# Kernel optimization log

Hardware: AMD Instinct MI355X
Metric: run time of the kernel (lower is better)

Reference implementation:

```python
import jax, jax.numpy as jnp
import numpy as np

B, N, HID, H, M = 4, 16384, 512, 8, 32
D = HID // H  # 64


def setup_inputs() -> dict:
    key = jax.random.key(0)
    ks = jax.random.split(key, 8)
    s = 0.02
    return {
        "x": jax.random.normal(ks[0], (B, N, HID), jnp.float32),
        "wkv": jax.random.normal(ks[1], (2 * HID, HID), jnp.float32) * s,
        "bkv": jnp.zeros((2 * HID,), jnp.float32),
        "wtq": jax.random.normal(ks[2], (H, M, D), jnp.float32) * s,
        "alpha1": jnp.ones((H,), jnp.float32),
        "mix1_w": jax.random.normal(ks[3], (H * M, H * M), jnp.float32) * (1.0 / np.sqrt(H * M)),
        "ln1_w": jnp.ones((D,), jnp.float32),
        "ln1_b": jnp.zeros((D,), jnp.float32),
        "wqkv": jax.random.normal(ks[4], (3 * HID, HID), jnp.float32) * s,
        "wout": jax.random.normal(ks[5], (HID, HID), jnp.float32) * s,
        "bout": jnp.zeros((HID,), jnp.float32),
    }


def _layernorm(x, w, b, eps=1e-5):
    mu = x.mean(-1, keepdims=True)
    var = ((x - mu) ** 2).mean(-1, keepdims=True)
    return (x - mu) * jax.lax.rsqrt(var + eps) * w + b


def reference(x, wkv, bkv, wtq, alpha1, mix1_w, ln1_w, ln1_b, wqkv, wout, bout):
    # key/value projection: [B, N, 2*HID]
    kv = x @ wkv.T + bkv
    xk, xv = jnp.split(kv, 2, axis=-1)
    xk = xk.reshape(B, N, H, D).transpose(0, 2, 1, 3)  # b h n d
    xv = xv.reshape(B, N, H, D).transpose(0, 2, 1, 3)
    # slice scores + 1x1 conv head-mixing over the (H*M) channel dim
    scores = jnp.einsum('hmd,bhnd->bhmn', wtq, xk)
    scores = jnp.einsum('oc,bcn->bon', mix1_w, scores.reshape(B, H * M, N)).reshape(B, H, M, N)
    # softmax over the slice dim M (dim=-2)
    sw = jax.nn.softmax(scores * alpha1[:, None, None], axis=-2)  # b h m n
    # weighted reduction to slice tokens, normalized by total weight per slice
    tok = jnp.einsum('bhmn,bhnd->bhmd', sw, xv)
    tok = tok / (sw.sum(axis=-1, keepdims=True) + 1e-5)
    tok = _layernorm(tok, ln1_w, ln1_b)
    tok = tok.transpose(0, 2, 1, 3).reshape(B, M, HID)  # b m (h d)
    # small inner MHA over the M=32 slice tokens
    qkv = tok @ wqkv.T
    q, k, v = jnp.split(qkv, 3, axis=-1)
    q = q.reshape(B, M, H, D).transpose(0, 2, 1, 3)
    k = k.reshape(B, M, H, D).transpose(0, 2, 1, 3)
    v = v.reshape(B, M, H, D).transpose(0, 2, 1, 3)
    dots = jnp.einsum('bhqd,bhkd->bhqk', q, k) * (D ** -0.5)
    attn = jax.nn.softmax(dots, axis=-1)
    out_tok = jnp.einsum('bhqk,bhkd->bhqd', attn, v)
    # broadcast slice tokens back to the N points via slice weights
    out = jnp.einsum('bhmd,bhmn->bhnd', out_tok, sw)
    out = out.transpose(0, 2, 1, 3).reshape(B, N, HID)
    out = out @ wout.T + bout
    return (out, sw, alpha1[:, None, None], jnp.zeros((H, M), jnp.float32), attn)
```

## Files before the change

kernel.cpp:

```cpp
#include <hip/hip_runtime.h>
#include <hip/hip_bf16.h>

#define B_ 4
#define N_ 16384
#define HID_ 512
#define H_ 8
#define M_ 32
#define D_ 64
#define HM_ 256

typedef __hip_bfloat16 bf16;
typedef __bf16 bf16x8 __attribute__((ext_vector_type(8)));
typedef float f32x4 __attribute__((ext_vector_type(4)));

__device__ __forceinline__ void gl_lds16(const bf16* g, bf16* l) {
    __builtin_amdgcn_global_load_lds(
        (const __attribute__((address_space(1))) void*)g,
        (__attribute__((address_space(3))) void*)l, 16, 0, 0);
}

__device__ __forceinline__ int xcd_swz(int lin, int nwg) {
    return (lin & 7) * (nwg >> 3) + (lin >> 3);
}

__device__ __forceinline__ void stage_tile_lin(const bf16* __restrict__ G, long long r0,
        int kk, int ld, bf16* lds, int t) {
    const int l = t & 63, w = t >> 6;
    const int srow = l >> 3;
    const int skel = (l & 7) * 8;
#pragma unroll
    for (int j = 0; j < 4; ++j) {
        int q = j * 4 + w;
        gl_lds16(G + (r0 + q * 8 + srow) * (long long)ld + kk + skel, lds + q * 512);
    }
}

__device__ __forceinline__ void stage_tile_sw(const bf16* __restrict__ G, long long r0,
        int kk, int ld, bf16* lds, int t) {
    const int l = t & 63, w = t >> 6;
    const int srow = l >> 3;
    const int skel = ((l & 7) ^ srow) * 8;
#pragma unroll
    for (int j = 0; j < 4; ++j) {
        int q = j * 4 + w;
        gl_lds16(G + (r0 + q * 8 + srow) * (long long)ld + kk + skel, lds + q * 512);
    }
}

__device__ __forceinline__ void mfma_half(const bf16* As, const bf16* Bs,
        int l, int wm, int wn, f32x4 acc[4][4]) {
#pragma unroll
    for (int ks = 0; ks < 64; ks += 32) {
        bf16x8 af[4], bfr[4];
#pragma unroll
        for (int mf = 0; mf < 4; ++mf)
            af[mf] = *(const bf16x8*)(As + (wm * 64 + mf * 16 + (l & 15)) * 64 + ks + (l >> 4) * 8);
#pragma unroll
        for (int nf = 0; nf < 4; ++nf)
            bfr[nf] = *(const bf16x8*)(Bs + (wn * 64 + nf * 16 + (l & 15)) * 64 + ks + (l >> 4) * 8);
#pragma unroll
        for (int mf = 0; mf < 4; ++mf)
#pragma unroll
            for (int nf = 0; nf < 4; ++nf)
                acc[mf][nf] = __builtin_amdgcn_mfma_f32_16x16x32_bf16(af[mf], bfr[nf], acc[mf][nf], 0, 0, 0);
    }
}

__device__ __forceinline__ void mfma_half_sw(const bf16* As, const bf16* Bs,
        int l, int wm, int wn, f32x4 acc[4][4]) {
    const int l15 = l & 15;
    const int xsw = (l & 7) * 8;
    const int kq = (l >> 4) * 8;
#pragma unroll
    for (int ks = 0; ks < 64; ks += 32) {
        const int ko = (ks + kq) ^ xsw;
        bf16x8 af[4], bfr[4];
#pragma unroll
        for (int mf = 0; mf < 4; ++mf)
            af[mf] = *(const bf16x8*)(As + (wm * 64 + mf * 16 + l15) * 64 + ko);
#pragma unroll
        for (int nf = 0; nf < 4; ++nf)
            bfr[nf] = *(const bf16x8*)(Bs + (wn * 64 + nf * 16 + l15) * 64 + ko);
#pragma unroll
        for (int mf = 0; mf < 4; ++mf)
#pragma unroll
            for (int nf = 0; nf < 4; ++nf)
                acc[mf][nf] = __builtin_amdgcn_mfma_f32_16x16x32_bf16(af[mf], bfr[nf], acc[mf][nf], 0, 0, 0);
    }
}

__device__ __forceinline__ void mfma_core(
        const bf16* __restrict__ Ag, const bf16* __restrict__ Bg,
        long long arow0, int bcol0, int lda, int ldb, int kiters,
        bf16* As, bf16* Bs, f32x4 acc[4][4]) {
    const int t = threadIdx.x;
    const int l = t & 63, w = t >> 6;
    const int wm = w >> 1, wn = w & 1;
    for (int kt = 0; kt < kiters; ++kt) {
        const int kk = kt * 64;
        stage_tile_lin(Ag, arow0, kk, lda, As, t);
        stage_tile_lin(Bg, bcol0, kk, ldb, Bs, t);
        __syncthreads();
        mfma_half(As, Bs, l, wm, wn, acc);
        __syncthreads();
    }
}

template<int NT>
__device__ __forceinline__ void gemm_cnt(
        const bf16* __restrict__ Ag, const bf16* __restrict__ Bg,
        long long arow0, int bcol0, int lda, int ldb,
        bf16 (*As)[8192], bf16 (*Bs)[8192], f32x4 acc[4][4]) {
    const int t = threadIdx.x;
    const int l = t & 63, w = t >> 6;
    const int wm = w >> 1, wn = w & 1;
    stage_tile_sw(Ag, arow0, 0, lda, As[0], t);
    stage_tile_sw(Bg, bcol0, 0, ldb, Bs[0], t);
#pragma unroll
    for (int kt = 0; kt < NT; ++kt) {
        const int cur = kt & 1;
        if (kt + 1 < NT) {
            stage_tile_sw(Ag, arow0, (kt + 1) * 64, lda, As[cur ^ 1], t);
            stage_tile_sw(Bg, bcol0, (kt + 1) * 64, ldb, Bs[cur ^ 1], t);
            asm volatile("s_waitcnt vmcnt(8)" ::: "memory");
        } else {
            asm volatile("s_waitcnt vmcnt(0)" ::: "memory");
        }
        __builtin_amdgcn_s_barrier();
        mfma_half_sw(As[cur], Bs[cur], l, wm, wn, acc);
        __builtin_amdgcn_s_barrier();
    }
}

__global__ __launch_bounds__(256) void k_cast4(const float* __restrict__ s,
        ushort* __restrict__ d) {
    long long i = (long long)blockIdx.x * 256 + threadIdx.x;
    float4 v = reinterpret_cast<const float4*>(s)[i];
    ushort4 o;
    bf16 a0 = __float2bfloat16(v.x), a1 = __float2bfloat16(v.y);
    bf16 a2 = __float2bfloat16(v.z), a3 = __float2bfloat16(v.w);
    o.x = *(ushort*)&a0; o.y = *(ushort*)&a1; o.z = *(ushort*)&a2; o.w = *(ushort*)&a3;
    reinterpret_cast<ushort4*>(d)[i] = o;
}

__global__ __launch_bounds__(256) void k_wfused(const float* __restrict__ mix1,
        const float* __restrict__ wtq, float* __restrict__ wf) {
    const int idx = blockIdx.x * 256 + threadIdx.x;
    const int o = idx >> 9, k = idx & 511;
    const int h = k >> 6, dd = k & 63;
    float s = 0.f;
#pragma unroll
    for (int m = 0; m < 32; ++m)
        s += mix1[(long long)o * 256 + h * 32 + m] * wtq[((long long)h * 32 + m) * 64 + dd];
    wf[(long long)o * 512 + k] = s;
}

__global__ __launch_bounds__(256) void k_wsc(const float* __restrict__ wf,
        const float* __restrict__ wkv, const float* __restrict__ bkv,
        const float* __restrict__ alpha1, bf16* __restrict__ wv_sc,
        float* __restrict__ bias768) {
    __shared__ float wfrow[512];
    __shared__ float red[256];
    const int o = blockIdx.x, t = threadIdx.x;
    wfrow[t] = wf[(long long)o * 512 + t];
    wfrow[t + 256] = wf[(long long)o * 512 + 256 + t];
    __syncthreads();
    const float al = alpha1[o >> 5];
    float a0 = 0.f, a1 = 0.f;
    for (int c = 0; c < 512; ++c) {
        float wv = wfrow[c];
        a0 += wv * wkv[(long long)c * 512 + t];
        a1 += wv * wkv[(long long)c * 512 + t + 256];
    }
    wv_sc[(long long)(512 + o) * 512 + t] = __float2bfloat16(a0 * al);
    wv_sc[(long long)(512 + o) * 512 + t + 256] = __float2bfloat16(a1 * al);
    float p = wfrow[t] * bkv[t] + wfrow[t + 256] * bkv[t + 256];
    red[t] = p; __syncthreads();
    for (int s = 128; s >= 1; s >>= 1) {
        if (t < s) red[t] += red[t + s];
        __syncthreads();
    }
    if (t == 0) bias768[512 + o] = red[0] * al;
    if (t < 2) bias768[o * 2 + t] = bkv[512 + o * 2 + t];
}

__global__ __launch_bounds__(256) void k12_mfma(const bf16* __restrict__ xb,
        const bf16* __restrict__ wv_sc, const float* __restrict__ bias768,
        bf16* __restrict__ xv, float* __restrict__ swout,
        bf16* __restrict__ sw_bt, float* __restrict__ part) {
    __shared__ __align__(16) bf16 As[2][8192];
    __shared__ __align__(16) bf16 Bs[2][8192];
    f32x4 acc[4][4];
#pragma unroll
    for (int i = 0; i < 4; ++i)
#pragma unroll
        for (int j = 0; j < 4; ++j) acc[i][j] = (f32x4)(0.0f);
    const int wg = xcd_swz(blockIdx.y * 6 + blockIdx.x, 3072);
    const int bx = wg % 6, by = wg / 6;
    const long long arow0 = (long long)by * 128;
    const int bcol0 = bx * 128;
    gemm_cnt<8>(xb, wv_sc, arow0, bcol0, 512, 512, As, Bs, acc);

    const int t = threadIdx.x;
    const int l = t & 63, w = t >> 6, wm = w >> 1, wn = w & 1;
    const int l15 = l & 15, lq = l >> 4;
#pragma unroll
    for (int nf = 0; nf < 4; ++nf) {
        float bv = bias768[bcol0 + wn * 64 + nf * 16 + l15];
#pragma unroll
        for (int mf = 0; mf < 4; ++mf)
#pragma unroll
            for (int r = 0; r < 4; ++r) acc[mf][nf][r] += bv;
    }

    if (bcol0 >= 512) {
#pragma unroll
        for (int mf = 0; mf < 4; ++mf)
#pragma unroll
            for (int r = 0; r < 4; ++r)
#pragma unroll
                for (int g = 0; g < 2; ++g) {
                    float v0 = acc[mf][2 * g][r], v1 = acc[mf][2 * g + 1][r];
                    float mx = fmaxf(v0, v1);
#pragma unroll
                    for (int mk = 1; mk <= 8; mk <<= 1) mx = fmaxf(mx, __shfl_xor(mx, mk));
                    float e0 = __expf(v0 - mx), e1 = __expf(v1 - mx);
                    float s = e0 + e1;
#pragma unroll
                    for (int mk = 1; mk <= 8; mk <<= 1) s += __shfl_xor(s, mk);
                    float ri = 1.f / s;
                    acc[mf][2 * g][r] = e0 * ri;
                    acc[mf][2 * g + 1][r] = e1 * ri;
                }
        {
            float* cpart = (float*)&As[0][0];
#pragma unroll
            for (int nf = 0; nf < 4; ++nf) {
                float ps = 0.f;
#pragma unroll
                for (int mf = 0; mf < 4; ++mf)
#pragma unroll
                    for (int r = 0; r < 4; ++r) ps += acc[mf][nf][r];
                ps += __shfl_xor(ps, 16);
                ps += __shfl_xor(ps, 32);
                if (lq == 0) cpart[wm * 128 + wn * 64 + nf * 16 + l15] = ps;
            }
            __syncthreads();
            if (t < 128)
                part[(long long)by * 256 + (bcol0 - 512) + t] = cpart[t] + cpart[128 + t];
        }
        const int b = (int)(arow0 >> 14);
        const int nbase = (int)(arow0 & 16383) + wm * 64;
#pragma unroll
        for (int mf = 0; mf < 4; ++mf) {
            long long rowb = arow0 + wm * 64 + mf * 16 + lq * 4;
#pragma unroll
            for (int nf = 0; nf < 4; ++nf) {
                int cglob = (bcol0 - 512) + wn * 64 + nf * 16 + l15;
                float4 v = {acc[mf][nf][0], acc[mf][nf][1], acc[mf][nf][2], acc[mf][nf][3]};
                *reinterpret_cast<float4*>(swout + ((long long)b * HM_ + cglob) * N_
                                           + nbase + mf * 16 + lq * 4) = v;
#pragma unroll
                for (int r = 0; r < 4; ++r)
                    sw_bt[(rowb + r) * 256 + cglob] = __float2bfloat16(acc[mf][nf][r]);
            }
        }
    } else {
#pragma unroll
        for (int mf = 0; mf < 4; ++mf) {
            long long rowb = arow0 + wm * 64 + mf * 16 + lq * 4;
#pragma unroll
            for (int nf = 0; nf < 4; ++nf) {
                int col = bcol0 + wn * 64 + nf * 16 + l15;
#pragma unroll
                for (int r = 0; r < 4; ++r)
                    xv[(rowb + r) * 512 + col] = __float2bfloat16(acc[mf][nf][r]);
            }
        }
    }
}

__global__ __launch_bounds__(256) void k3_tok(const bf16* __restrict__ sw_bt,
        const bf16* __restrict__ xv, float* __restrict__ tok_part) {
    __shared__ __align__(16) float smem[17408];
    float (*swsT)[36] = reinterpret_cast<float(*)[36]>(smem);
    bf16* xvs = reinterpret_cast<bf16*>(smem + 9216);
    const int t = threadIdx.x;
    const int chunk = blockIdx.x;
    const int bh = blockIdx.y;
    const int n0 = chunk * 256;
    const int b = bh >> 3, h = bh & 7;
    {
        const long long base = ((long long)(b * N_ + n0 + t)) * 256 + h * 32;
        const uint4* sp = reinterpret_cast<const uint4*>(sw_bt + base);
        uint4 qs[4] = {sp[0], sp[1], sp[2], sp[3]};
        const uint* qu = reinterpret_cast<const uint*>(qs);
#pragma unroll
        for (int j = 0; j < 16; ++j) {
            uint u = qu[j];
            swsT[t][2 * j] = __uint_as_float(u << 16);
            swsT[t][2 * j + 1] = __uint_as_float(u & 0xffff0000u);
        }
    }
    {
        const uint* xg = reinterpret_cast<const uint*>(xv + ((long long)b * N_ + n0) * 512 + h * 64);
        uint* xls = reinterpret_cast<uint*>(xvs);
#pragma unroll
        for (int p = 0; p < 32; ++p) {
            int idx = p * 256 + t;
            int nl = idx >> 5, prt = idx & 31;
            xls[nl * 32 + prt] = xg[(long long)nl * 256 + prt];
        }
    }
    __syncthreads();
    const int l = t & 63, w = t >> 6;
    const int nlh = l >> 5, mtile = (l >> 3) & 3, dtile = l & 7;
    const int m0 = mtile * 8, d0 = dtile * 8;
    float acc[8][8] = {};
    const int wbase = w * 64;
    for (int i = 0; i < 32; ++i) {
        int nl = wbase + i * 2 + nlh;
        float4 s0 = *reinterpret_cast<const float4*>(&swsT[nl][m0]);
        float4 s1 = *reinterpret_cast<const float4*>(&swsT[nl][m0 + 4]);
        uint4 xi = *reinterpret_cast<const uint4*>(&xvs[nl * 64 + d0]);
        float xvf[8];
        xvf[0] = __uint_as_float(xi.x << 16); xvf[1] = __uint_as_float(xi.x & 0xffff0000u);
        xvf[2] = __uint_as_float(xi.y << 16); xvf[3] = __uint_as_float(xi.y & 0xffff0000u);
        xvf[4] = __uint_as_float(xi.z << 16); xvf[5] = __uint_as_float(xi.z & 0xffff0000u);
        xvf[6] = __uint_as_float(xi.w << 16); xvf[7] = __uint_as_float(xi.w & 0xffff0000u);
        float sm[8] = {s0.x, s0.y, s0.z, s0.w, s1.x, s1.y, s1.z, s1.w};
#pragma unroll
        for (int mi = 0; mi < 8; ++mi)
#pragma unroll
            for (int di = 0; di < 8; ++di)
                acc[mi][di] += sm[mi] * xvf[di];
    }
    __syncthreads();
    float* red = smem;
    float* rb = red + (w * 2 + nlh) * 2048;
#pragma unroll
    for (int mi = 0; mi < 8; ++mi) {
        float4 lo = {acc[mi][0], acc[mi][1], acc[mi][2], acc[mi][3]};
        float4 hi = {acc[mi][4], acc[mi][5], acc[mi][6], acc[mi][7]};
        *reinterpret_cast<float4*>(&rb[(m0 + mi) * 64 + d0]) = lo;
        *reinterpret_cast<float4*>(&rb[(m0 + mi) * 64 + d0 + 4]) = hi;
    }
    __syncthreads();
#pragma unroll
    for (int pp = 0; pp < 2; ++pp) {
        int idx4 = pp * 1024 + t * 4;
        float4 s = {0.f, 0.f, 0.f, 0.f};
#pragma unroll
        for (int r = 0; r < 8; ++r) {
            float4 v = *reinterpret_cast<const float4*>(&red[r * 2048 + idx4]);
            s.x += v.x; s.y += v.y; s.z += v.z; s.w += v.w;
        }
        *reinterpret_cast<float4*>(&tok_part[((long long)bh * 64 + chunk) * 2048 + idx4]) = s;
    }
}

__global__ __launch_bounds__(64) void k4a_ln(const float* __restrict__ tok_part,
        const float* __restrict__ part, const float* __restrict__ ln_w,
        const float* __restrict__ ln_b, float* __restrict__ tok_ln) {
    const int bid = blockIdx.x;
    const int bh = bid >> 5, m = bid & 31;
    const int d = threadIdx.x;
    float s = 0.f;
    for (int ch = 0; ch < 64; ++ch)
        s += tok_part[(((long long)bh * 64 + ch) * 32 + m) * 64 + d];
    const int b = bid >> 8, c = bid & 255;
    float ssum = part[((long long)(b * 128 + d)) * 256 + c]
               + part[((long long)(b * 128 + 64 + d)) * 256 + c];
#pragma unroll
    for (int mk = 32; mk >= 1; mk >>= 1) ssum += __shfl_xor(ssum, mk, 64);
    float tokv = s / (ssum + 1e-5f);
    float mu = tokv;
#pragma unroll
    for (int mk = 32; mk >= 1; mk >>= 1) mu += __shfl_xor(mu, mk, 64);
    mu *= (1.f / 64.f);
    float df = tokv - mu;
    float var = df * df;
#pragma unroll
    for (int mk = 32; mk >= 1; mk >>= 1) var += __shfl_xor(var, mk, 64);
    var *= (1.f / 64.f);
    float y = df * rsqrtf(var + 1e-5f) * ln_w[d] + ln_b[d];
    const int bb = bh >> 3, h = bh & 7;
    tok_ln[((long long)bb * 32 + m) * 512 + h * 64 + d] = y;
}

__global__ __launch_bounds__(256) void k_wqT(const float* __restrict__ wq,
        float* __restrict__ wqT) {
    __shared__ float tile[32][33];
    const int k0 = blockIdx.x * 32;
    const int j0 = blockIdx.y * 32;
    const int tx = threadIdx.x & 31, ty = threadIdx.x >> 5;
#pragma unroll
    for (int r = 0; r < 32; r += 8)
        tile[ty + r][tx] = wq[(long long)(j0 + ty + r) * 512 + k0 + tx];
    __syncthreads();
#pragma unroll
    for (int r = 0; r < 32; r += 8)
        wqT[(long long)(k0 + ty + r) * 1536 + j0 + tx] = tile[tx][ty + r];
}

__global__ __launch_bounds__(256) void k4b_qkv(const float* __restrict__ tok_ln,
        const float* __restrict__ wqT, float* __restrict__ qkv) {
    const int j = (blockIdx.x % 6) * 256 + threadIdx.x;
    const int r0 = (blockIdx.x / 6) * 4;
    float a0 = 0, a1 = 0, a2 = 0, a3 = 0;
    for (int k = 0; k < 512; ++k) {
        float wv = wqT[(long long)k * 1536 + j];
        a0 += tok_ln[(r0 + 0) * 512 + k] * wv;
        a1 += tok_ln[(r0 + 1) * 512 + k] * wv;
        a2 += tok_ln[(r0 + 2) * 512 + k] * wv;
        a3 += tok_ln[(r0 + 3) * 512 + k] * wv;
    }
    qkv[(long long)(r0 + 0) * 1536 + j] = a0;
    qkv[(long long)(r0 + 1) * 1536 + j] = a1;
    qkv[(long long)(r0 + 2) * 1536 + j] = a2;
    qkv[(long long)(r0 + 3) * 1536 + j] = a3;
}

__global__ __launch_bounds__(256) void k4c_attn(const float* __restrict__ qkv,
        float* __restrict__ out_tok, float* __restrict__ attn_out) {
    __shared__ float qsT[64][33], ksT[64][33], vsT[64][33];
    __shared__ float att[32][33];
    __shared__ float rinv[32];
    const int t = threadIdx.x;
    const int bid = blockIdx.x;
    const int b = bid >> 3, h = bid & 7;
#pragma unroll
    for (int i = 0; i < 8; ++i) {
        int idx = i * 256 + t;
        int mi = idx >> 6, dd = idx & 63;
        long long base = ((long long)b * 32 + mi) * 1536 + h * 64 + dd;
        qsT[dd][mi] = qkv[base];
        ksT[dd][mi] = qkv[base + 512];
        vsT[dd][mi] = qkv[base + 1024];
    }
    __syncthreads();
#pragma unroll
    for (int i = 0; i < 4; ++i) {
        int idx = i * 256 + t;
        int qi = idx >> 5, ki = idx & 31;
        float s = 0.f;
#pragma unroll
        for (int dd = 0; dd < 64; ++dd) s += qsT[dd][qi] * ksT[dd][ki];
        att[qi][ki] = s * 0.125f;
    }
    __syncthreads();
    if (t < 32) {
        float mx = -1e30f;
        for (int k = 0; k < 32; ++k) mx = fmaxf(mx, att[t][k]);
        float sum = 0.f;
        for (int k = 0; k < 32; ++k) { float e = __expf(att[t][k] - mx); att[t][k] = e; sum += e; }
        rinv[t] = 1.f / sum;
    }
    __syncthreads();
#pragma unroll
    for (int i = 0; i < 4; ++i) {
        int idx = i * 256 + t;
        int qi = idx >> 5, ki = idx & 31;
        float a = att[qi][ki] * rinv[qi];
        att[qi][ki] = a;
        attn_out[(long long)bid * 1024 + qi * 32 + ki] = a;
    }
    __syncthreads();
#pragma unroll
    for (int i = 0; i < 8; ++i) {
        int idx = i * 256 + t;
        int qi = idx >> 6, dd = idx & 63;
        float s = 0.f;
#pragma unroll
        for (int ki = 0; ki < 32; ++ki) s += att[qi][ki] * vsT[dd][ki];
        out_tok[((long long)bid * 32 + qi) * 64 + dd] = s;
    }
}

__global__ __launch_bounds__(256) void k5_w2(const float* __restrict__ wout,
        const float* __restrict__ out_tok, bf16* __restrict__ W2) {
    const int bid = blockIdx.x;
    const int b = bid >> 9, o = bid & 511;
    const int t = threadIdx.x;
    const int h = t >> 5, m = t & 31;
    float s = 0.f;
#pragma unroll
    for (int dd = 0; dd < 64; ++dd)
        s += wout[(long long)o * 512 + h * 64 + dd]
           * out_tok[(((long long)b * 8 + h) * 32 + m) * 64 + dd];
    W2[(long long)bid * 256 + t] = __float2bfloat16(s);
}

__global__ __launch_bounds__(256) void k6_mfma(const bf16* __restrict__ sw_bt,
        const bf16* __restrict__ W2, const float* __restrict__ bout,
        float* __restrict__ out) {
    __shared__ bf16 As[128 * 64], Bs[128 * 64];
    f32x4 acc[4][4];
#pragma unroll
    for (int i = 0; i < 4; ++i)
#pragma unroll
        for (int j = 0; j < 4; ++j) acc[i][j] = (f32x4)(0.0f);
    const int wg = xcd_swz((blockIdx.z * 128 + blockIdx.y) * 4 + blockIdx.x, 2048);
    const int bx = wg & 3, by = (wg >> 2) & 127, bz = wg >> 9;
    const long long arow0 = (long long)by * 128;
    const int bcol0 = bx * 128;
    mfma_core(sw_bt + (long long)bz * N_ * 256, W2 + (long long)bz * 512 * 256,
              arow0, bcol0, 256, 256, 4, As, Bs, acc);
    const int l = threadIdx.x & 63, w = threadIdx.x >> 6;
    const int wm = w >> 1, wn = w & 1;
#pragma unroll
    for (int mf = 0; mf < 4; ++mf) {
#pragma unroll
        for (int nf = 0; nf < 4; ++nf) {
            int col = bcol0 + wn * 64 + nf * 16 + (l & 15);
            float bv = bout[col];
#pragma unroll
            for (int r = 0; r < 4; ++r) {
                long long row = arow0 + wm * 64 + mf * 16 + (l >> 4) * 4 + r;
                out[((long long)bz * N_ + row) * 512 + col] = acc[mf][nf][r] + bv;
            }
        }
    }
}

__global__ void k_misc(const float* __restrict__ alpha1,
        float* __restrict__ outA, float* __restrict__ outZ) {
    int t = threadIdx.x;
    if (t < 8) outA[t] = alpha1[t];
    outZ[t] = 0.f;
}

extern "C" void kernel_launch(void* const* d_in, const int* in_sizes, int n_in,
                              void* d_out, int out_size, void* d_ws, size_t ws_size,
                              hipStream_t stream) {
    const float* x      = (const float*)d_in[0];
    const float* wkv    = (const float*)d_in[1];
    const float* bkv    = (const float*)d_in[2];
    const float* wtq    = (const float*)d_in[3];
    const float* alpha1 = (const float*)d_in[4];
    const float* mix1_w = (const float*)d_in[5];
    const float* ln1_w  = (const float*)d_in[6];
    const float* ln1_b  = (const float*)d_in[7];
    const float* wqkv   = (const float*)d_in[8];
    const float* wout   = (const float*)d_in[9];
    const float* bout   = (const float*)d_in[10];

    float* out    = (float*)d_out;
    float* swout  = out + 33554432LL;
    float* alphaO = out + 50331648LL;
    float* zerosO = out + 50331656LL;
    float* attnO  = out + 50331912LL;

    char* ws = (char*)d_ws;
    bf16*  xb        = (bf16*)(ws);
    float* wqkvT     = (float*)(ws);
    float* wf_f32    = (float*)(ws + 35651584LL);
    float* part      = (float*)(ws + 67108864LL);
    bf16*  sw_bt     = (bf16*)(ws + 100663296LL);
    bf16*  xv        = (bf16*)(ws + 134217728LL);
    float* tok_part  = (float*)(ws + 201326592LL);
    float* tok_ln    = (float*)(ws + 218107904LL);
    float* qkv       = (float*)(ws + 218370048LL);
    float* out_tok   = (float*)(ws + 219156480LL);
    bf16*  W2b       = (bf16*)(ws + 219418624LL);
    bf16*  wv_sc     = (bf16*)(ws + 220467200LL);
    float* bias768   = (float*)(ws + 221253632LL);

    k_cast4<<<256, 256, 0, stream>>>(wkv + 262144, (ushort*)wv_sc);
    k_wfused<<<512, 256, 0, stream>>>(mix1_w, wtq, wf_f32);
    k_wsc<<<256, 256, 0, stream>>>(wf_f32, wkv, bkv, alpha1, wv_sc, bias768);
    k_cast4<<<32768, 256, 0, stream>>>(x, (ushort*)xb);
    k12_mfma<<<dim3(6, 512), 256, 0, stream>>>(xb, wv_sc, bias768, xv, swout, sw_bt, part);
    k_wqT<<<dim3(16, 48), 256, 0, stream>>>(wqkv, wqkvT);
    k3_tok<<<dim3(64, 32), 256, 0, stream>>>(sw_bt, xv, tok_part);
    k4a_ln<<<1024, 64, 0, stream>>>(tok_part, part, ln1_w, ln1_b, tok_ln);
    k4b_qkv<<<192, 256, 0, stream>>>(tok_ln, wqkvT, qkv);
    k4c_attn<<<32, 256, 0, stream>>>(qkv, out_tok, attnO);
    k5_w2<<<2048, 256, 0, stream>>>(wout, out_tok, W2b);
    k6_mfma<<<dim3(4, 128, 4), 256, 0, stream>>>(sw_bt, W2b, bout, out);
    k_misc<<<1, 256, 0, stream>>>(alpha1, alphaO, zerosO);
}
```

Measured before the change: 337.1 us.

## Enlarge k12 GEMM tile to 256 rows with 512-thread blocks

The fused KV/score GEMM kernel now uses 256x128 output tiles computed by eight waves instead of 128x128 with four waves. Each B tile is reused across twice as many rows, and the grid is halved. The staging loaders, the vmcnt wait count, the partial column-sum reduction and the downstream layernorm kernel's part indexing are all updated to match. It doubles LDS use for A and halves the number of workgroups, which may lower occupancy. The epilogue code that still derives wm from w>>1 needs checking for correctness with eight waves.

```diff
diff --git a/kernel.cpp b/kernel.cpp
--- a/kernel.cpp
+++ b/kernel.cpp
@@ -35,14 +35,25 @@
     }
 }
 
-__device__ __forceinline__ void stage_tile_sw(const bf16* __restrict__ G, long long r0,
+__device__ __forceinline__ void stage_a_sw(const bf16* __restrict__ G, long long r0,
         int kk, int ld, bf16* lds, int t) {
     const int l = t & 63, w = t >> 6;
     const int srow = l >> 3;
     const int skel = ((l & 7) ^ srow) * 8;
 #pragma unroll
     for (int j = 0; j < 4; ++j) {
-        int q = j * 4 + w;
+        int q = j * 8 + w;
+        gl_lds16(G + (r0 + q * 8 + srow) * (long long)ld + kk + skel, lds + q * 512);
+    }
+}
+__device__ __forceinline__ void stage_b_sw(const bf16* __restrict__ G, long long r0,
+        int kk, int ld, bf16* lds, int t) {
+    const int l = t & 63, w = t >> 6;
+    const int srow = l >> 3;
+    const int skel = ((l & 7) ^ srow) * 8;
+#pragma unroll
+    for (int j = 0; j < 2; ++j) {
+        int q = j * 8 + w;
         gl_lds16(G + (r0 + q * 8 + srow) * (long long)ld + kk + skel, lds + q * 512);
     }
 }
@@ -107,22 +118,22 @@
 }
 
 template<int NT>
-__device__ __forceinline__ void gemm_cnt(
+__device__ __forceinline__ void gemm_cnt256(
         const bf16* __restrict__ Ag, const bf16* __restrict__ Bg,
         long long arow0, int bcol0, int lda, int ldb,
-        bf16 (*As)[8192], bf16 (*Bs)[8192], f32x4 acc[4][4]) {
+        bf16 (*As)[16384], bf16 (*Bs)[8192], f32x4 acc[4][4]) {
     const int t = threadIdx.x;
     const int l = t & 63, w = t >> 6;
     const int wm = w >> 1, wn = w & 1;
-    stage_tile_sw(Ag, arow0, 0, lda, As[0], t);
-    stage_tile_sw(Bg, bcol0, 0, ldb, Bs[0], t);
+    stage_a_sw(Ag, arow0, 0, lda, As[0], t);
+    stage_b_sw(Bg, bcol0, 0, ldb, Bs[0], t);
 #pragma unroll
     for (int kt = 0; kt < NT; ++kt) {
         const int cur = kt & 1;
         if (kt + 1 < NT) {
-            stage_tile_sw(Ag, arow0, (kt + 1) * 64, lda, As[cur ^ 1], t);
-            stage_tile_sw(Bg, bcol0, (kt + 1) * 64, ldb, Bs[cur ^ 1], t);
-            asm volatile("s_waitcnt vmcnt(8)" ::: "memory");
+            stage_a_sw(Ag, arow0, (kt + 1) * 64, lda, As[cur ^ 1], t);
+            stage_b_sw(Bg, bcol0, (kt + 1) * 64, ldb, Bs[cur ^ 1], t);
+            asm volatile("s_waitcnt vmcnt(6)" ::: "memory");
         } else {
             asm volatile("s_waitcnt vmcnt(0)" ::: "memory");
         }
@@ -184,22 +195,22 @@
     if (t < 2) bias768[o * 2 + t] = bkv[512 + o * 2 + t];
 }
 
-__global__ __launch_bounds__(256) void k12_mfma(const bf16* __restrict__ xb,
+__global__ __launch_bounds__(512) void k12_mfma(const bf16* __restrict__ xb,
         const bf16* __restrict__ wv_sc, const float* __restrict__ bias768,
         bf16* __restrict__ xv, float* __restrict__ swout,
         bf16* __restrict__ sw_bt, float* __restrict__ part) {
-    __shared__ __align__(16) bf16 As[2][8192];
+    __shared__ __align__(16) bf16 As[2][16384];
     __shared__ __align__(16) bf16 Bs[2][8192];
     f32x4 acc[4][4];
 #pragma unroll
     for (int i = 0; i < 4; ++i)
 #pragma unroll
         for (int j = 0; j < 4; ++j) acc[i][j] = (f32x4)(0.0f);
-    const int wg = xcd_swz(blockIdx.y * 6 + blockIdx.x, 3072);
+    const int wg = xcd_swz(blockIdx.y * 6 + blockIdx.x, 1536);
     const int bx = wg % 6, by = wg / 6;
-    const long long arow0 = (long long)by * 128;
+    const long long arow0 = (long long)by * 256;
     const int bcol0 = bx * 128;
-    gemm_cnt<8>(xb, wv_sc, arow0, bcol0, 512, 512, As, Bs, acc);
+    gemm_cnt256<8>(xb, wv_sc, arow0, bcol0, 512, 512, As, Bs, acc);
 
     const int t = threadIdx.x;
     const int l = t & 63, w = t >> 6, wm = w >> 1, wn = w & 1;
@@ -247,7 +258,8 @@
             }
             __syncthreads();
             if (t < 128)
-                part[(long long)by * 256 + (bcol0 - 512) + t] = cpart[t] + cpart[128 + t];
+                part[(long long)by * 256 + (bcol0 - 512) + t]
+                    = cpart[t] + cpart[128 + t] + cpart[256 + t] + cpart[384 + t];
         }
         const int b = (int)(arow0 >> 14);
         const int nbase = (int)(arow0 & 16383) + wm * 64;
@@ -369,8 +381,7 @@
     for (int ch = 0; ch < 64; ++ch)
         s += tok_part[(((long long)bh * 64 + ch) * 32 + m) * 64 + d];
     const int b = bid >> 8, c = bid & 255;
-    float ssum = part[((long long)(b * 128 + d)) * 256 + c]
-               + part[((long long)(b * 128 + 64 + d)) * 256 + c];
+    float ssum = part[((long long)(b * 64 + d)) * 256 + c];
 #pragma unroll
     for (int mk = 32; mk >= 1; mk >>= 1) ssum += __shfl_xor(ssum, mk, 64);
     float tokv = s / (ssum + 1e-5f);
@@ -570,7 +581,7 @@
     k_wfused<<<512, 256, 0, stream>>>(mix1_w, wtq, wf_f32);
     k_wsc<<<256, 256, 0, stream>>>(wf_f32, wkv, bkv, alpha1, wv_sc, bias768);
     k_cast4<<<32768, 256, 0, stream>>>(x, (ushort*)xb);
-    k12_mfma<<<dim3(6, 512), 256, 0, stream>>>(xb, wv_sc, bias768, xv, swout, sw_bt, part);
+    k12_mfma<<<dim3(6, 256), 512, 0, stream>>>(xb, wv_sc, bias768, xv, swout, sw_bt, part);
     k_wqT<<<dim3(16, 48), 256, 0, stream>>>(wqkv, wqkvT);
     k3_tok<<<dim3(64, 32), 256, 0, stream>>>(sw_bt, xv, tok_part);
     k4a_ln<<<1024, 64, 0, stream>>>(tok_part, part, ln1_w, ln1_b, tok_ln);
```

Result: slower. 351.3 us (+4.2%).
